# Performance work log

Hardware: AMD Instinct MI355X
Metric: run time of the kernel (lower is better)

The kernel has to match this reference:

```python
import jax, jax.numpy as jnp
import numpy as np

N_ATOMS = 131072
N_EDGES = 524288
N_MOLS = 2048
D = 128      # n_atom_basis
F = 128      # n_filters
G = 50       # n_gaussians
T = 3        # interaction blocks
CUTOFF = 5.0
LOG2 = float(np.log(2.0))


def ssp(x):
    # shifted softplus: ln(0.5*e^x + 0.5) = softplus(x) - ln 2
    return jax.nn.softplus(x) - LOG2


def setup_inputs() -> dict:
    key = jax.random.key(0)
    ks = jax.random.split(key, 20)
    s = 0.05
    z = jax.random.randint(ks[0], (N_ATOMS,), 1, 100, dtype=jnp.int32)
    xyz = jax.random.normal(ks[1], (N_ATOMS, 3), dtype=jnp.float32) * 3.0
    a0 = jax.random.randint(ks[2], (N_EDGES,), 0, N_ATOMS, dtype=jnp.int32)
    off = jax.random.randint(ks[3], (N_EDGES,), 1, N_ATOMS, dtype=jnp.int32)
    a = jnp.stack([a0, (a0 + off) % N_ATOMS], axis=1)  # distinct endpoints
    mol_id = jnp.sort(jax.random.randint(ks[4], (N_ATOMS,), 0, N_MOLS, dtype=jnp.int32))
    emb = (jax.random.normal(ks[5], (100, D)) * s).at[0].set(0.0)  # padding_idx=0
    return dict(
        xyz=xyz,
        emb=emb,
        fw1=jax.random.normal(ks[6], (T, G, F)) * s,
        fb1=jnp.zeros((T, F)),
        fw2=jax.random.normal(ks[7], (T, F, F)) * s,
        fb2=jnp.zeros((T, F)),
        win=jax.random.normal(ks[8], (T, D, F)) * s,
        wout1=jax.random.normal(ks[9], (T, F, D)) * s,
        bout1=jnp.zeros((T, D)),
        wout2=jax.random.normal(ks[10], (T, D, D)) * s,
        bout2=jnp.zeros((T, D)),
        wa1=jax.random.normal(ks[11], (D, D // 2)) * s,
        ba1=jnp.zeros((D // 2,)),
        wa2=jax.random.normal(ks[12], (D // 2, 1)) * s,
        ba2=jnp.zeros((1,)),
        z=z, a=a, mol_id=mol_id,
    )


def reference(xyz, emb, fw1, fb1, fw2, fb2, win, wout1, bout1, wout2, bout2,
              wa1, ba1, wa2, ba2, z, a, mol_id):
    r = emb[z]                                            # [N, D] atom embeddings
    # edge distances: e = ||xyz[a0] - xyz[a1]||  -> [E, 1]
    d = jnp.sqrt(((xyz[a[:, 0]] - xyz[a[:, 1]]) ** 2).sum(-1))[:, None]
    # Gaussian smearing on [0, cutoff]
    offsets = jnp.linspace(0.0, CUTOFF, G)
    width = offsets[1] - offsets[0]
    g = jnp.exp((-0.5 / width ** 2) * (d - offsets) ** 2)  # [E, G]
    # smooth cosine cutoff (cutoff_soft)
    C = 0.5 * (jnp.cos(d * jnp.pi / CUTOFF) + 1.0)          # [E, 1]
    for t in range(T):
        # continuous filter network on edge features
        W = ssp(g @ fw1[t] + fb1[t]) @ fw2[t] + fb2[t]      # [E, F]
        W = W * C
        h = r @ win[t]                                      # in2f, no bias [N, F]
        # symmetric gather-filter-scatter over undirected edge list
        y = jnp.zeros_like(h)
        y = y.at[a[:, 0]].add(h[a[:, 1]] * W)
        y = y.at[a[:, 1]].add(h[a[:, 0]] * W)
        dr = ssp(y @ wout1[t] + bout1[t]) @ wout2[t] + bout2[t]
        r = r + dr                                          # residual update
    # atomwise energy head
    r = ssp(r @ wa1 + ba1) @ wa2 + ba2                      # [N, 1]
    # per-molecule sum pooling (torch.split + sum)
    return jax.ops.segment_sum(r, mol_id, num_segments=N_MOLS)  # [N_MOLS, 1]
```

## Files before the change

kernel.cpp:

```cpp
#include <hip/hip_runtime.h>
#include <hip/hip_bf16.h>

#define N_ATOMS 131072
#define N_EDGES 524288
#define N_MOLS  2048
#define DD      128
#define FF      128
#define GG      50
#define TT      3

typedef __hip_bfloat16 bf16;
typedef __attribute__((ext_vector_type(8))) short short8;
typedef __attribute__((ext_vector_type(4))) float floatx4;

__device__ __forceinline__ float b2f(bf16 v) { return __bfloat162float(v); }
__device__ __forceinline__ bf16  f2b(float v) { return __float2bfloat16(v); }

__device__ __forceinline__ unsigned short f2bu(float f) {
    unsigned u = __float_as_uint(f);
    u += 0x7fff + ((u >> 16) & 1);
    return (unsigned short)(u >> 16);
}
__device__ __forceinline__ bf16 f2b_fast(float f) {
    union { unsigned short u; bf16 b; } c; c.u = f2bu(f); return c.b;
}
__device__ __forceinline__ unsigned int pk2(float lo, float hi) {
    return ((unsigned)f2bu(hi) << 16) | f2bu(lo);
}

__device__ __forceinline__ float2 up2(unsigned int u) {
    float2 f;
    f.x = __uint_as_float(u << 16);
    f.y = __uint_as_float(u & 0xffff0000u);
    return f;
}

__device__ __forceinline__ float sspf(float x) {
    float e = __expf(-fabsf(x));
    return fmaxf(x, 0.f) + __logf(1.f + e) - 0.69314718056f;
}

__device__ __forceinline__ void fma8(float* ac, uint4 wv, uint4 hv) {
    float2 w0 = up2(wv.x), h0 = up2(hv.x);
    float2 w1 = up2(wv.y), h1 = up2(hv.y);
    float2 w2 = up2(wv.z), h2 = up2(hv.z);
    float2 w3 = up2(wv.w), h3 = up2(hv.w);
    ac[0] = fmaf(w0.x, h0.x, ac[0]); ac[1] = fmaf(w0.y, h0.y, ac[1]);
    ac[2] = fmaf(w1.x, h1.x, ac[2]); ac[3] = fmaf(w1.y, h1.y, ac[3]);
    ac[4] = fmaf(w2.x, h2.x, ac[4]); ac[5] = fmaf(w2.y, h2.y, ac[5]);
    ac[6] = fmaf(w3.x, h3.x, ac[6]); ac[7] = fmaf(w3.y, h3.y, ac[7]);
}

template <int NCT>
__device__ __forceinline__ void mfma_half(const bf16* A, const bf16* B,
                                          floatx4 (&acc)[2][NCT],
                                          int kA, int wave, int q, int ln) {
#pragma unroll
    for (int k0 = 0; k0 < 64; k0 += 32) {
        short8 a0 = *(const short8*)(A + (wave * 32 + ln) * 136 + kA + k0 + q * 8);
        short8 a1 = *(const short8*)(A + (wave * 32 + 16 + ln) * 136 + kA + k0 + q * 8);
#pragma unroll
        for (int ct = 0; ct < NCT; ct++) {
            short8 b = *(const short8*)(B + (ct * 16 + ln) * 72 + k0 + q * 8);
            acc[0][ct] = __builtin_amdgcn_mfma_f32_16x16x32_bf16(a0, b, acc[0][ct], 0, 0, 0);
            acc[1][ct] = __builtin_amdgcn_mfma_f32_16x16x32_bf16(a1, b, acc[1][ct], 0, 0, 0);
        }
    }
}

template <int NCT>
__device__ __forceinline__ void mfma64(const bf16* A, const bf16* B,
                                       floatx4 (&acc)[NCT],
                                       int kA, int wave, int q, int ln) {
#pragma unroll
    for (int k0 = 0; k0 < 64; k0 += 32) {
        short8 a = *(const short8*)(A + (wave * 16 + ln) * 136 + kA + k0 + q * 8);
#pragma unroll
        for (int ct = 0; ct < NCT; ct++) {
            short8 b = *(const short8*)(B + (ct * 16 + ln) * 72 + k0 + q * 8);
            acc[ct] = __builtin_amdgcn_mfma_f32_16x16x32_bf16(a, b, acc[ct], 0, 0, 0);
        }
    }
}

__device__ __forceinline__ void stage_b(bf16* B, const bf16* WT, int k0,
                                        int nrows, int ldk, int tid) {
    for (int i = tid; i < nrows * 8; i += 256) {
        int n = i >> 3, kc = i & 7;
        *(short8*)(B + n * 72 + kc * 8) =
            *(const short8*)(WT + n * ldk + k0 + kc * 8);
    }
}

__global__ __launch_bounds__(256) void k_init(const float* __restrict__ emb,
                                              const int* __restrict__ z,
                                              float* __restrict__ r) {
    int idx = blockIdx.x * 256 + threadIdx.x;
    int atom = idx >> 7, col = idx & 127;
    r[idx] = emb[z[atom] * DD + col];
}

__global__ __launch_bounds__(256) void k_dist(const float* __restrict__ xyz,
                                              const int* __restrict__ a,
                                              float* __restrict__ dArr,
                                              float* __restrict__ cArr,
                                              float* __restrict__ molE) {
    int e = blockIdx.x * 256 + threadIdx.x;
    if (e < N_MOLS) molE[e] = 0.f;
    int A0 = a[2 * e], A1 = a[2 * e + 1];
    float dx = xyz[3 * A0]     - xyz[3 * A1];
    float dy = xyz[3 * A0 + 1] - xyz[3 * A1 + 1];
    float dz = xyz[3 * A0 + 2] - xyz[3 * A1 + 2];
    float d = sqrtf(dx * dx + dy * dy + dz * dz);
    dArr[e] = d;
    cArr[e] = 0.5f * (__cosf(d * 0.6283185307179586f) + 1.f);
}

__global__ __launch_bounds__(256) void k_wt(const float* __restrict__ fw1,
                                            const float* __restrict__ fw2,
                                            const float* __restrict__ win,
                                            const float* __restrict__ wout1,
                                            const float* __restrict__ wout2,
                                            const float* __restrict__ wa1,
                                            bf16* __restrict__ fw1T, bf16* __restrict__ fw2T,
                                            bf16* __restrict__ winT, bf16* __restrict__ wout1T,
                                            bf16* __restrict__ wout2T, bf16* __restrict__ wa1T) {
    int idx = blockIdx.x * 256 + threadIdx.x;
    if (idx < 3 * 128 * 64) {
        int t = idx / 8192, j = idx % 8192;
        int n = j >> 6, k = j & 63;
        fw1T[idx] = (k < GG) ? f2b(fw1[t * GG * FF + k * FF + n]) : f2b(0.f);
        return;
    }
    idx -= 3 * 128 * 64;
    if (idx < 3 * 16384) { int t = idx / 16384, j = idx % 16384; int n = j >> 7, k = j & 127;
        fw2T[idx] = f2b(fw2[t * 16384 + k * 128 + n]); return; }
    idx -= 3 * 16384;
    if (idx < 3 * 16384) { int t = idx / 16384, j = idx % 16384; int n = j >> 7, k = j & 127;
        winT[idx] = f2b(win[t * 16384 + k * 128 + n]); return; }
    idx -= 3 * 16384;
    if (idx < 3 * 16384) { int t = idx / 16384, j = idx % 16384; int n = j >> 7, k = j & 127;
        wout1T[idx] = f2b(wout1[t * 16384 + k * 128 + n]); return; }
    idx -= 3 * 16384;
    if (idx < 3 * 16384) { int t = idx / 16384, j = idx % 16384; int n = j >> 7, k = j & 127;
        wout2T[idx] = f2b(wout2[t * 16384 + k * 128 + n]); return; }
    idx -= 3 * 16384;
    if (idx < 64 * 128) { int n = idx >> 7, k = idx & 127;
        wa1T[idx] = f2b(wa1[k * 64 + n]); return; }
}

__global__ __launch_bounds__(256) void k_zero(int* __restrict__ p, int n) {
    int i = blockIdx.x * 256 + threadIdx.x;
    if (i < n) p[i] = 0;
}

__global__ __launch_bounds__(256) void k_count2(const int* __restrict__ a,
                                                int* __restrict__ cntA,
                                                int* __restrict__ cnt1,
                                                float* __restrict__ molE) {
    int e = blockIdx.x * 256 + threadIdx.x;
    if (e < N_MOLS) molE[e] = 0.f;
    atomicAdd(&cntA[a[2 * e]], 1);
    atomicAdd(&cnt1[a[2 * e + 1]], 1);
}

__global__ __launch_bounds__(256) void k_scan1(const int* __restrict__ counts,
                                               int* __restrict__ bsum) {
    __shared__ int red[256];
    int tid = threadIdx.x;
    int i0 = blockIdx.x * 512 + tid * 2;
    red[tid] = counts[i0] + counts[i0 + 1];
    __syncthreads();
    for (int off = 128; off > 0; off >>= 1) {
        if (tid < off) red[tid] += red[tid + off];
        __syncthreads();
    }
    if (tid == 0) bsum[blockIdx.x] = red[0];
}

__global__ __launch_bounds__(256) void k_scan2(int* __restrict__ bsum,
                                               int* __restrict__ ptr) {
    __shared__ int v[256];
    int tid = threadIdx.x;
    v[tid] = bsum[tid];
    __syncthreads();
    if (tid == 0) {
        int acc = 0;
        for (int i = 0; i < 256; i++) { int t = v[i]; v[i] = acc; acc += t; }
        ptr[N_ATOMS] = acc;
    }
    __syncthreads();
    bsum[tid] = v[tid];
}

__global__ __launch_bounds__(256) void k_scan3(int* __restrict__ counts,
                                               const int* __restrict__ bsum,
                                               int* __restrict__ ptr) {
    __shared__ int red[256];
    int tid = threadIdx.x;
    int i0 = blockIdx.x * 512 + tid * 2;
    int c0 = counts[i0], c1 = counts[i0 + 1];
    int s = c0 + c1;
    red[tid] = s;
    __syncthreads();
    for (int off = 1; off < 256; off <<= 1) {
        int t = (tid >= off) ? red[tid - off] : 0;
        __syncthreads();
        red[tid] += t;
        __syncthreads();
    }
    int base = bsum[blockIdx.x] + red[tid] - s;
    ptr[i0] = base;
    ptr[i0 + 1] = base + c0;
    counts[i0] = base;
    counts[i0 + 1] = base + c0;
}

__global__ __launch_bounds__(256) void k_permA(const float* __restrict__ xyz,
                                               const int* __restrict__ a,
                                               int* __restrict__ cursorA,
                                               int* __restrict__ cursor1,
                                               float* __restrict__ dAp,
                                               float* __restrict__ cAp,
                                               int* __restrict__ a1s,
                                               int* __restrict__ adj1) {
    int e = blockIdx.x * 256 + threadIdx.x;
    int A0 = a[2 * e], A1 = a[2 * e + 1];
    float dx = xyz[3 * A0]     - xyz[3 * A1];
    float dy = xyz[3 * A0 + 1] - xyz[3 * A1 + 1];
    float dz = xyz[3 * A0 + 2] - xyz[3 * A1 + 2];
    float d = sqrtf(dx * dx + dy * dy + dz * dz);
    int newe = atomicAdd(&cursorA[A0], 1);
    dAp[newe] = d;
    cAp[newe] = 0.5f * (__cosf(d * 0.6283185307179586f) + 1.f);
    a1s[newe] = A1;
    int slot = atomicAdd(&cursor1[A1], 1);
    adj1[2 * slot] = newe;
    adj1[2 * slot + 1] = A0;
}

struct SmemHE {
    bf16 A[64][136];
    bf16 B[128][72];
    float dS[64], cS[64], b1S[128], b2S[128];
};

__device__ __forceinline__ void h_part(SmemHE& sm, int blk,
                                       const float* __restrict__ r,
                                       const bf16* __restrict__ winT_t,
                                       bf16* __restrict__ h) {
    int tid = threadIdx.x, n0 = blk * 64;
    for (int i = tid; i < 64 * 32; i += 256) {
        int row = i >> 5, c4 = (i & 31) * 4;
        float4 v = *(const float4*)(r + (size_t)(n0 + row) * DD + c4);
        uint2 p; p.x = pk2(v.x, v.y); p.y = pk2(v.z, v.w);
        *(uint2*)(&sm.A[row][c4]) = p;
    }
    stage_b(&sm.B[0][0], winT_t, 0, 128, 128, tid);
    __syncthreads();
    int wave = tid >> 6, lane = tid & 63, q = lane >> 4, ln = lane & 15;
    floatx4 acc[8];
#pragma unroll
    for (int j = 0; j < 8; j++) acc[j] = (floatx4){0.f, 0.f, 0.f, 0.f};
    mfma64<8>(&sm.A[0][0], &sm.B[0][0], acc, 0, wave, q, ln);
    __syncthreads();
    stage_b(&sm.B[0][0], winT_t, 64, 128, 128, tid);
    __syncthreads();
    mfma64<8>(&sm.A[0][0], &sm.B[0][0], acc, 64, wave, q, ln);
#pragma unroll
    for (int ct = 0; ct < 8; ct++)
#pragma unroll
        for (int rg = 0; rg < 4; rg++) {
            int row = wave * 16 + q * 4 + rg, col = ct * 16 + ln;
            sm.A[row][col] = f2b_fast(acc[ct][rg]);
        }
    __syncthreads();
    for (int i = tid; i < 64 * 16; i += 256) {
        int row = i >> 4, seg = i & 15;
        *(uint4*)(h + (size_t)(n0 + row) * FF + seg * 8) =
            *(const uint4*)(&sm.A[row][seg * 8]);
    }
}

__device__ __forceinline__ void edge_part(SmemHE& sm, int blk,
                                          const float* __restrict__ dAp,
                                          const float* __restrict__ cAp,
                                          const bf16* __restrict__ fw1T_t,
                                          const float* __restrict__ fb1_t,
                                          const bf16* __restrict__ fw2T_t,
                                          const float* __restrict__ fb2_t,
                                          bf16* __restrict__ Wt) {
    int tid = threadIdx.x, e0 = blk * 64;
    if (tid < 64) { sm.dS[tid] = dAp[e0 + tid]; sm.cS[tid] = cAp[e0 + tid]; }
    if (tid < 128) { sm.b1S[tid] = fb1_t[tid]; sm.b2S[tid] = fb2_t[tid]; }
    stage_b(&sm.B[0][0], fw1T_t, 0, 128, 64, tid);
    __syncthreads();
    const float width = 5.0f / 49.0f;
    const float coeff = -0.5f / (width * width);
    for (int idx = tid; idx < 64 * 32; idx += 256) {
        int i = idx >> 5, kp = (idx & 31) * 2;
        float d = sm.dS[i];
        float t0 = d - (float)kp * width;
        float t1 = d - (float)(kp + 1) * width;
        float v0 = (kp < GG)     ? __expf(coeff * t0 * t0) : 0.f;
        float v1 = (kp + 1 < GG) ? __expf(coeff * t1 * t1) : 0.f;
        *(unsigned int*)(&sm.A[i][kp]) = pk2(v0, v1);
    }
    __syncthreads();
    int wave = tid >> 6, lane = tid & 63, q = lane >> 4, ln = lane & 15;
    floatx4 acc[8];
#pragma unroll
    for (int j = 0; j < 8; j++) acc[j] = (floatx4){0.f, 0.f, 0.f, 0.f};
    mfma64<8>(&sm.A[0][0], &sm.B[0][0], acc, 0, wave, q, ln);
#pragma unroll
    for (int ct = 0; ct < 8; ct++)
#pragma unroll
        for (int rg = 0; rg < 4; rg++) {
            int row = wave * 16 + q * 4 + rg, col = ct * 16 + ln;
            sm.A[row][col] = f2b_fast(sspf(acc[ct][rg] + sm.b1S[col]));
        }
    __syncthreads();
    stage_b(&sm.B[0][0], fw2T_t, 0, 128, 128, tid);
    __syncthreads();
#pragma unroll
    for (int j = 0; j < 8; j++) acc[j] = (floatx4){0.f, 0.f, 0.f, 0.f};
    mfma64<8>(&sm.A[0][0], &sm.B[0][0], acc, 0, wave, q, ln);
    __syncthreads();
    stage_b(&sm.B[0][0], fw2T_t, 64, 128, 128, tid);
    __syncthreads();
    mfma64<8>(&sm.A[0][0], &sm.B[0][0], acc, 64, wave, q, ln);
#pragma unroll
    for (int ct = 0; ct < 8; ct++)
#pragma unroll
        for (int rg = 0; rg < 4; rg++) {
            int row = wave * 16 + q * 4 + rg, col = ct * 16 + ln;
            sm.A[row][col] = f2b_fast((acc[ct][rg] + sm.b2S[col]) * sm.cS[row]);
        }
    __syncthreads();
    for (int i = tid; i < 64 * 16; i += 256) {
        int row = i >> 4, seg = i & 15;
        *(uint4*)(Wt + (size_t)(e0 + row) * FF + seg * 8) =
            *(const uint4*)(&sm.A[row][seg * 8]);
    }
}

__global__ __launch_bounds__(256, 4) void k_he(const float* __restrict__ r,
                                               const bf16* __restrict__ winT_t,
                                               bf16* __restrict__ h,
                                               const float* __restrict__ dAp,
                                               const float* __restrict__ cAp,
                                               const bf16* __restrict__ fw1T_t,
                                               const float* __restrict__ fb1_t,
                                               const bf16* __restrict__ fw2T_t,
                                               const float* __restrict__ fb2_t,
                                               bf16* __restrict__ Wt) {
    __shared__ SmemHE sm;
    int bi = blockIdx.x;
    if (bi % 5 == 0)
        h_part(sm, bi / 5, r, winT_t, h);
    else
        edge_part(sm, bi - bi / 5 - 1, dAp, cAp, fw1T_t, fb1_t, fw2T_t, fb2_t, Wt);
}

__global__ __launch_bounds__(256, 5) void k_gather_node64(const int* __restrict__ baseA,
                                                          const int* __restrict__ a1s,
                                                          const int* __restrict__ ptr1,
                                                          const int* __restrict__ adj1,
                                                          const bf16* __restrict__ Wt,
                                                          const bf16* __restrict__ h,
                                                          const bf16* __restrict__ wout1T_t,
                                                          const float* __restrict__ bo1_t,
                                                          const bf16* __restrict__ wout2T_t,
                                                          const float* __restrict__ bo2_t,
                                                          float* __restrict__ r) {
    __shared__ __align__(16) bf16 A[64][136];
    __shared__ __align__(16) bf16 B[64][72];
    __shared__ float b1S[128], b2S[128];
    int tid = threadIdx.x, n0 = blockIdx.x * 64;
    if (tid < 128) { b1S[tid] = bo1_t[tid]; b2S[tid] = bo2_t[tid]; }
    stage_b(&B[0][0], wout1T_t, 0, 64, 128, tid);
    int wave = tid >> 6, lane = tid & 63;
    int seg = lane & 15;
    int rg  = lane >> 4;
    for (int k = 0; k < 16; k++) {
        int row = wave * 16 + k;
        int atom = n0 + row;
        int s0 = baseA[atom] + rg, e0v = baseA[atom + 1];
        int s1 = ptr1[atom] + rg, e1v = ptr1[atom + 1];
        int o0 = (s0 < e0v) ? a1s[s0] : 0;
        int2 eo = (s1 < e1v) ? *(const int2*)(adj1 + 2 * s1) : make_int2(0, 0);
        float ac[8];
#pragma unroll
        for (int j = 0; j < 8; j++) ac[j] = 0.f;
        while (s0 < e0v || s1 < e1v) {
            bool p0 = s0 < e0v, p1 = s1 < e1v;
            uint4 wv0, hv0, wv1, hv1;
            if (p0) {
                wv0 = *(const uint4*)(Wt + (size_t)s0 * FF + seg * 8);
                hv0 = *(const uint4*)(h + (size_t)o0 * FF + seg * 8);
            }
            if (p1) {
                wv1 = *(const uint4*)(Wt + (size_t)eo.x * FF + seg * 8);
                hv1 = *(const uint4*)(h + (size_t)eo.y * FF + seg * 8);
            }
            int s0n = s0 + 4, s1n = s1 + 4;
            int o0n = (s0n < e0v) ? a1s[s0n] : 0;
            int2 eon = (s1n < e1v) ? *(const int2*)(adj1 + 2 * s1n) : make_int2(0, 0);
            if (p0) fma8(ac, wv0, hv0);
            if (p1) fma8(ac, wv1, hv1);
            s0 = s0n; s1 = s1n; o0 = o0n; eo = eon;
        }
#pragma unroll
        for (int j = 0; j < 8; j++) {
            float v = ac[j];
            v += __shfl_down(v, 32);
            v += __shfl_down(v, 16);
            ac[j] = v;
        }
        if (rg == 0) {
            uint4 o;
            o.x = pk2(ac[0], ac[1]);
            o.y = pk2(ac[2], ac[3]);
            o.z = pk2(ac[4], ac[5]);
            o.w = pk2(ac[6], ac[7]);
            *(uint4*)(&A[row][seg * 8]) = o;
        }
    }
    __syncthreads();
    int q = lane >> 4, ln = lane & 15;
    floatx4 acc[8];
#pragma unroll
    for (int j = 0; j < 8; j++) acc[j] = (floatx4){0.f, 0.f, 0.f, 0.f};
    mfma64<4>(&A[0][0], &B[0][0], *(floatx4(*)[4])(&acc[0]), 0, wave, q, ln);
    __syncthreads();
    stage_b(&B[0][0], wout1T_t + 64 * 128, 0, 64, 128, tid);
    __syncthreads();
    mfma64<4>(&A[0][0], &B[0][0], *(floatx4(*)[4])(&acc[4]), 0, wave, q, ln);
    __syncthreads();
    stage_b(&B[0][0], wout1T_t, 64, 64, 128, tid);
    __syncthreads();
    mfma64<4>(&A[0][0], &B[0][0], *(floatx4(*)[4])(&acc[0]), 64, wave, q, ln);
    __syncthreads();
    stage_b(&B[0][0], wout1T_t + 64 * 128, 64, 64, 128, tid);
    __syncthreads();
    mfma64<4>(&A[0][0], &B[0][0], *(floatx4(*)[4])(&acc[4]), 64, wave, q, ln);
#pragma unroll
    for (int cc = 0; cc < 8; cc++)
#pragma unroll
        for (int rgi = 0; rgi < 4; rgi++) {
            int row = wave * 16 + q * 4 + rgi;
            int col = (cc >> 2) * 64 + (cc & 3) * 16 + ln;
            A[row][col] = f2b_fast(sspf(acc[cc][rgi] + b1S[col]));
        }
    __syncthreads();
    stage_b(&B[0][0], wout2T_t, 0, 64, 128, tid);
    __syncthreads();
#pragma unroll
    for (int j = 0; j < 8; j++) acc[j] = (floatx4){0.f, 0.f, 0.f, 0.f};
    mfma64<4>(&A[0][0], &B[0][0], *(floatx4(*)[4])(&acc[0]), 0, wave, q, ln);
    __syncthreads();
    stage_b(&B[0][0], wout2T_t + 64 * 128, 0, 64, 128, tid);
    __syncthreads();
    mfma64<4>(&A[0][0], &B[0][0], *(floatx4(*)[4])(&acc[4]), 0, wave, q, ln);
    __syncthreads();
    stage_b(&B[0][0], wout2T_t, 64, 64, 128, tid);
    __syncthreads();
    mfma64<4>(&A[0][0], &B[0][0], *(floatx4(*)[4])(&acc[0]), 64, wave, q, ln);
    __syncthreads();
    stage_b(&B[0][0], wout2T_t + 64 * 128, 64, 64, 128, tid);
    __syncthreads();
    mfma64<4>(&A[0][0], &B[0][0], *(floatx4(*)[4])(&acc[4]), 64, wave, q, ln);
#pragma unroll
    for (int cc = 0; cc < 8; cc++)
#pragma unroll
        for (int rgi = 0; rgi < 4; rgi++) {
            int row = wave * 16 + q * 4 + rgi;
            int col = (cc >> 2) * 64 + (cc & 3) * 16 + ln;
            size_t off = (size_t)(n0 + row) * DD + col;
            r[off] += acc[cc][rgi] + b2S[col];
        }
}

__global__ __launch_bounds__(256) void k_h(const float* __restrict__ r,
                                           const bf16* __restrict__ winT_t,
                                           bf16* __restrict__ h,
                                           float* __restrict__ y) {
    __shared__ __align__(16) bf16 A[128][136];
    __shared__ __align__(16) bf16 B[128][72];
    int tid = threadIdx.x, n0 = blockIdx.x * 128;
    for (int i = tid; i < 128 * 32; i += 256) {
        int row = i >> 5, c4 = (i & 31) * 4;
        float4 v = *(const float4*)(r + (size_t)(n0 + row) * DD + c4);
        A[row][c4]     = f2b(v.x);
        A[row][c4 + 1] = f2b(v.y);
        A[row][c4 + 2] = f2b(v.z);
        A[row][c4 + 3] = f2b(v.w);
        *(float4*)(y + (size_t)(n0 + row) * FF + c4) = (float4){0.f, 0.f, 0.f, 0.f};
    }
    stage_b(&B[0][0], winT_t, 0, 128, 128, tid);
    __syncthreads();
    int wave = tid >> 6, lane = tid & 63, q = lane >> 4, ln = lane & 15;
    floatx4 acc[2][8];
#pragma unroll
    for (int i = 0; i < 2; i++)
#pragma unroll
        for (int j = 0; j < 8; j++) acc[i][j] = (floatx4){0.f, 0.f, 0.f, 0.f};
    mfma_half<8>(&A[0][0], &B[0][0], acc, 0, wave, q, ln);
    __syncthreads();
    stage_b(&B[0][0], winT_t, 64, 128, 128, tid);
    __syncthreads();
    mfma_half<8>(&A[0][0], &B[0][0], acc, 64, wave, q, ln);
#pragma unroll
    for (int rt = 0; rt < 2; rt++)
#pragma unroll
        for (int ct = 0; ct < 8; ct++)
#pragma unroll
            for (int rg = 0; rg < 4; rg++) {
                int row = wave * 32 + rt * 16 + q * 4 + rg, col = ct * 16 + ln;
                h[(size_t)(n0 + row) * FF + col] = f2b(acc[rt][ct][rg]);
            }
}

__global__ __launch_bounds__(256) void k_edge(const float* __restrict__ dArr,
                                              const float* __restrict__ cArr,
                                              const int* __restrict__ a,
                                              const bf16* __restrict__ fw1T_t,
                                              const float* __restrict__ fb1_t,
                                              const bf16* __restrict__ fw2T_t,
                                              const float* __restrict__ fb2_t,
                                              const bf16* __restrict__ h,
                                              float* __restrict__ y) {
    __shared__ __align__(16) bf16 A[128][136];
    __shared__ __align__(16) bf16 B[128][72];
    __shared__ float dS[128], cS[128], b1S[128], b2S[128];
    __shared__ int a0S[128], a1S[128];
    int tid = threadIdx.x, e0 = blockIdx.x * 128;
    if (tid < 128) {
        int e = e0 + tid;
        dS[tid] = dArr[e]; cS[tid] = cArr[e];
        a0S[tid] = a[2 * e]; a1S[tid] = a[2 * e + 1];
        b1S[tid] = fb1_t[tid]; b2S[tid] = fb2_t[tid];
    }
    stage_b(&B[0][0], fw1T_t, 0, 128, 64, tid);
    __syncthreads();
    const float width = 5.0f / 49.0f;
    const float coeff = -0.5f / (width * width);
    for (int idx = tid; idx < 128 * 64; idx += 256) {
        int i = idx >> 6, k = idx & 63;
        float v = 0.f;
        if (k < GG) { float t = dS[i] - (float)k * width; v = __expf(coeff * t * t); }
        A[i][k] = f2b(v);
    }
    __syncthreads();
    int wave = tid >> 6, lane = tid & 63, q = lane >> 4, ln = lane & 15;
    floatx4 acc[2][8];
#pragma unroll
    for (int i = 0; i < 2; i++)
#pragma unroll
        for (int j = 0; j < 8; j++) acc[i][j] = (floatx4){0.f, 0.f, 0.f, 0.f};
    mfma_half<8>(&A[0][0], &B[0][0], acc, 0, wave, q, ln);
#pragma unroll
    for (int rt = 0; rt < 2; rt++)
#pragma unroll
        for (int ct = 0; ct < 8; ct++)
#pragma unroll
            for (int rg = 0; rg < 4; rg++) {
                int row = wave * 32 + rt * 16 + q * 4 + rg, col = ct * 16 + ln;
                A[row][col] = f2b(sspf(acc[rt][ct][rg] + b1S[col]));
            }
    __syncthreads();
    stage_b(&B[0][0], fw2T_t, 0, 128, 128, tid);
    __syncthreads();
#pragma unroll
    for (int i = 0; i < 2; i++)
#pragma unroll
        for (int j = 0; j < 8; j++) acc[i][j] = (floatx4){0.f, 0.f, 0.f, 0.f};
    mfma_half<8>(&A[0][0], &B[0][0], acc, 0, wave, q, ln);
    __syncthreads();
    stage_b(&B[0][0], fw2T_t, 64, 128, 128, tid);
    __syncthreads();
    mfma_half<8>(&A[0][0], &B[0][0], acc, 64, wave, q, ln);
#pragma unroll
    for (int rt = 0; rt < 2; rt++)
#pragma unroll
        for (int ct = 0; ct < 8; ct++)
#pragma unroll
            for (int rg = 0; rg < 4; rg++) {
                int row = wave * 32 + rt * 16 + q * 4 + rg, col = ct * 16 + ln;
                float w = (acc[rt][ct][rg] + b2S[col]) * cS[row];
                int A0 = a0S[row], A1 = a1S[row];
                float h0 = b2f(h[A0 * FF + col]);
                float h1 = b2f(h[A1 * FF + col]);
                atomicAdd(&y[A0 * FF + col], h1 * w);
                atomicAdd(&y[A1 * FF + col], h0 * w);
            }
}

__global__ __launch_bounds__(256) void k_node(const float* __restrict__ y,
                                              const bf16* __restrict__ wout1T_t,
                                              const float* __restrict__ bo1_t,
                                              const bf16* __restrict__ wout2T_t,
                                              const float* __restrict__ bo2_t,
                                              float* __restrict__ r) {
    __shared__ __align__(16) bf16 A[128][136];
    __shared__ __align__(16) bf16 B[128][72];
    __shared__ float b1S[128], b2S[128];
    int tid = threadIdx.x, n0 = blockIdx.x * 128;
    if (tid < 128) { b1S[tid] = bo1_t[tid]; b2S[tid] = bo2_t[tid]; }
    for (int idx = tid; idx < 128 * 128; idx += 256) {
        int row = idx >> 7, col = idx & 127;
        A[row][col] = f2b(y[(size_t)(n0 + row) * FF + col]);
    }
    stage_b(&B[0][0], wout1T_t, 0, 128, 128, tid);
    __syncthreads();
    int wave = tid >> 6, lane = tid & 63, q = lane >> 4, ln = lane & 15;
    floatx4 acc[2][8];
#pragma unroll
    for (int i = 0; i < 2; i++)
#pragma unroll
        for (int j = 0; j < 8; j++) acc[i][j] = (floatx4){0.f, 0.f, 0.f, 0.f};
    mfma_half<8>(&A[0][0], &B[0][0], acc, 0, wave, q, ln);
    __syncthreads();
    stage_b(&B[0][0], wout1T_t, 64, 128, 128, tid);
    __syncthreads();
    mfma_half<8>(&A[0][0], &B[0][0], acc, 64, wave, q, ln);
#pragma unroll
    for (int rt = 0; rt < 2; rt++)
#pragma unroll
        for (int ct = 0; ct < 8; ct++)
#pragma unroll
            for (int rg = 0; rg < 4; rg++) {
                int row = wave * 32 + rt * 16 + q * 4 + rg, col = ct * 16 + ln;
                A[row][col] = f2b(sspf(acc[rt][ct][rg] + b1S[col]));
            }
    __syncthreads();
    stage_b(&B[0][0], wout2T_t, 0, 128, 128, tid);
    __syncthreads();
#pragma unroll
    for (int i = 0; i < 2; i++)
#pragma unroll
        for (int j = 0; j < 8; j++) acc[i][j] = (floatx4){0.f, 0.f, 0.f, 0.f};
    mfma_half<8>(&A[0][0], &B[0][0], acc, 0, wave, q, ln);
    __syncthreads();
    stage_b(&B[0][0], wout2T_t, 64, 128, 128, tid);
    __syncthreads();
    mfma_half<8>(&A[0][0], &B[0][0], acc, 64, wave, q, ln);
#pragma unroll
    for (int rt = 0; rt < 2; rt++)
#pragma unroll
        for (int ct = 0; ct < 8; ct++)
#pragma unroll
            for (int rg = 0; rg < 4; rg++) {
                int row = wave * 32 + rt * 16 + q * 4 + rg, col = ct * 16 + ln;
                size_t off = (size_t)(n0 + row) * DD + col;
                r[off] += acc[rt][ct][rg] + b2S[col];
            }
}

__global__ __launch_bounds__(256) void k_head(const float* __restrict__ r,
                                              const bf16* __restrict__ wa1T,
                                              const float* __restrict__ ba1,
                                              const float* __restrict__ wa2,
                                              const float* __restrict__ ba2,
                                              const int* __restrict__ mol,
                                              float* __restrict__ molE) {
    __shared__ __align__(16) bf16 A[128][136];
    __shared__ __align__(16) bf16 B[64][72];
    __shared__ __align__(16) bf16 U[128][72];
    __shared__ float wa2S[64], ba1S[64];
    int tid = threadIdx.x, n0 = blockIdx.x * 128;
    if (tid < 64) { wa2S[tid] = wa2[tid]; ba1S[tid] = ba1[tid]; }
    for (int i = tid; i < 128 * 32; i += 256) {
        int row = i >> 5, c4 = (i & 31) * 4;
        float4 v = *(const float4*)(r + (size_t)(n0 + row) * DD + c4);
        uint2 p; p.x = pk2(v.x, v.y); p.y = pk2(v.z, v.w);
        *(uint2*)(&A[row][c4]) = p;
    }
    stage_b(&B[0][0], wa1T, 0, 64, 128, tid);
    __syncthreads();
    int wave = tid >> 6, lane = tid & 63, q = lane >> 4, ln = lane & 15;
    floatx4 acc[2][4];
#pragma unroll
    for (int i = 0; i < 2; i++)
#pragma unroll
        for (int j = 0; j < 4; j++) acc[i][j] = (floatx4){0.f, 0.f, 0.f, 0.f};
    mfma_half<4>(&A[0][0], &B[0][0], acc, 0, wave, q, ln);
    __syncthreads();
    stage_b(&B[0][0], wa1T, 64, 64, 128, tid);
    __syncthreads();
    mfma_half<4>(&A[0][0], &B[0][0], acc, 64, wave, q, ln);
#pragma unroll
    for (int rt = 0; rt < 2; rt++)
#pragma unroll
        for (int ct = 0; ct < 4; ct++)
#pragma unroll
            for (int rg = 0; rg < 4; rg++) {
                int row = wave * 32 + rt * 16 + q * 4 + rg, col = ct * 16 + ln;
                U[row][col] = f2b_fast(acc[rt][ct][rg] + ba1S[col]);
            }
    __syncthreads();
    if (tid < 128) {
        float s = ba2[0];
#pragma unroll
        for (int j = 0; j < 64; j++) s += sspf(b2f(U[tid][j])) * wa2S[j];
        atomicAdd(&molE[mol[n0 + tid]], s);
    }
}

__global__ __launch_bounds__(256) void k_out(const float* __restrict__ molE,
                                             float* __restrict__ out) {
    int i = blockIdx.x * 256 + threadIdx.x;
    out[i] = molE[i];
}

extern "C" void kernel_launch(void* const* d_in, const int* in_sizes, int n_in,
                              void* d_out, int out_size, void* d_ws, size_t ws_size,
                              hipStream_t stream) {
    const float* xyz   = (const float*)d_in[0];
    const float* emb   = (const float*)d_in[1];
    const float* fw1   = (const float*)d_in[2];
    const float* fb1   = (const float*)d_in[3];
    const float* fw2   = (const float*)d_in[4];
    const float* fb2   = (const float*)d_in[5];
    const float* win   = (const float*)d_in[6];
    const float* wout1 = (const float*)d_in[7];
    const float* bout1 = (const float*)d_in[8];
    const float* wout2 = (const float*)d_in[9];
    const float* bout2 = (const float*)d_in[10];
    const float* wa1   = (const float*)d_in[11];
    const float* ba1   = (const float*)d_in[12];
    const float* wa2   = (const float*)d_in[13];
    const float* ba2   = (const float*)d_in[14];
    const int*  z     = (const int*)d_in[15];
    const int*  a     = (const int*)d_in[16];
    const int*  mol   = (const int*)d_in[17];

    char* ws = (char*)d_ws;
    float* r    = (float*)ws; ws += (size_t)N_ATOMS * DD * 4;
    bf16*  h    = (bf16*) ws; ws += (size_t)N_ATOMS * FF * 2;
    float* molE = (float*)ws; ws += (size_t)N_MOLS * 4;
    float* dAp  = (float*)ws; ws += (size_t)N_EDGES * 4;
    float* cAp  = (float*)ws; ws += (size_t)N_EDGES * 4;
    bf16*  fw1T   = (bf16*)ws; ws += 3 * 128 * 64 * 2;
    bf16*  fw2T   = (bf16*)ws; ws += 3 * 128 * 128 * 2;
    bf16*  winT   = (bf16*)ws; ws += 3 * 128 * 128 * 2;
    bf16*  wout1T = (bf16*)ws; ws += 3 * 128 * 128 * 2;
    bf16*  wout2T = (bf16*)ws; ws += 3 * 128 * 128 * 2;
    bf16*  wa1T   = (bf16*)ws; ws += 64 * 128 * 2;
    char*  csr_base = ws;
    int*   baseA   = (int*)ws; ws += 524320;
    int*   ptr1    = (int*)ws; ws += 524320;
    int*   cursorA = (int*)ws; ws += (size_t)N_ATOMS * 4;
    int*   cursor1 = (int*)ws; ws += (size_t)N_ATOMS * 4;
    int*   a1s     = (int*)ws; ws += (size_t)N_EDGES * 4;
    int*   adj1    = (int*)ws; ws += (size_t)2 * N_EDGES * 4;
    int*   bsumA   = (int*)ws; ws += 1024;
    int*   bsum1   = (int*)ws; ws += 1024;
    bf16*  Wt      = (bf16*)ws; ws += (size_t)N_EDGES * FF * 2;
    size_t need = (size_t)(ws - (char*)d_ws);

    k_init<<<N_ATOMS * DD / 256, 256, 0, stream>>>(emb, z, r);
    k_wt<<<896, 256, 0, stream>>>(fw1, fw2, win, wout1, wout2, wa1,
                                  fw1T, fw2T, winT, wout1T, wout2T, wa1T);

    if (ws_size >= need) {
        k_zero<<<(N_ATOMS + 255) / 256, 256, 0, stream>>>(cursorA, N_ATOMS);
        k_zero<<<(N_ATOMS + 255) / 256, 256, 0, stream>>>(cursor1, N_ATOMS);
        k_count2<<<N_EDGES / 256, 256, 0, stream>>>(a, cursorA, cursor1, molE);
        k_scan1<<<256, 256, 0, stream>>>(cursorA, bsumA);
        k_scan2<<<1, 256, 0, stream>>>(bsumA, baseA);
        k_scan3<<<256, 256, 0, stream>>>(cursorA, bsumA, baseA);
        k_scan1<<<256, 256, 0, stream>>>(cursor1, bsum1);
        k_scan2<<<1, 256, 0, stream>>>(bsum1, ptr1);
        k_scan3<<<256, 256, 0, stream>>>(cursor1, bsum1, ptr1);
        k_permA<<<N_EDGES / 256, 256, 0, stream>>>(xyz, a, cursorA, cursor1,
                                                   dAp, cAp, a1s, adj1);
        for (int t = 0; t < TT; t++) {
            k_he<<<N_ATOMS / 64 + N_EDGES / 64, 256, 0, stream>>>(
                r, winT + t * 16384, h, dAp, cAp,
                fw1T + t * 8192, fb1 + t * FF,
                fw2T + t * 16384, fb2 + t * FF, Wt);
            k_gather_node64<<<N_ATOMS / 64, 256, 0, stream>>>(
                baseA, a1s, ptr1, adj1, Wt, h,
                wout1T + t * 16384, bout1 + t * DD,
                wout2T + t * 16384, bout2 + t * DD, r);
        }
    } else {
        float* y = (float*)csr_base;
        k_dist<<<N_EDGES / 256, 256, 0, stream>>>(xyz, a, dAp, cAp, molE);
        for (int t = 0; t < TT; t++) {
            k_h<<<N_ATOMS / 128, 256, 0, stream>>>(r, winT + t * 16384, h, y);
            k_edge<<<N_EDGES / 128, 256, 0, stream>>>(dAp, cAp, a,
                                                      fw1T + t * 8192, fb1 + t * FF,
                                                      fw2T + t * 16384, fb2 + t * FF, h, y);
            k_node<<<N_ATOMS / 128, 256, 0, stream>>>(y, wout1T + t * 16384, bout1 + t * DD,
                                                      wout2T + t * 16384, bout2 + t * DD, r);
        }
    }
    k_head<<<N_ATOMS / 128, 256, 0, stream>>>(r, wa1T, ba1, wa2, ba2, mol, molE);
    k_out<<<N_MOLS / 256, 256, 0, stream>>>(molE, (float*)d_out);
}
```

Measured before the change: 1.054 ms.

## Store residual state in bf16 and process two atoms per gather iteration

The residual atom state r is now held in bf16 instead of fp32, which halves its memory traffic in init, the h GEMM, the node update and the head, and removes the per-kernel fp32-to-bf16 packing. The gather/node kernel also processes two atoms at once in its neighbor loop, interleaving their edge streams to raise memory-level parallelism. The cost is that residual accumulation is rounded to bf16 on every block, which may affect accuracy, and that the unrolled loop uses more registers.

After: 993.9 us. 1.06x faster.

```diff
diff --git a/kernel.cpp b/kernel.cpp
--- a/kernel.cpp
+++ b/kernel.cpp
@@ -94,10 +94,16 @@
 
 __global__ __launch_bounds__(256) void k_init(const float* __restrict__ emb,
                                               const int* __restrict__ z,
-                                              float* __restrict__ r) {
+                                              bf16* __restrict__ rb) {
     int idx = blockIdx.x * 256 + threadIdx.x;
-    int atom = idx >> 7, col = idx & 127;
-    r[idx] = emb[z[atom] * DD + col];
+    int atom = idx >> 4, seg = idx & 15;
+    const float* src = emb + (size_t)z[atom] * DD + seg * 8;
+    float4 v0 = *(const float4*)(src);
+    float4 v1 = *(const float4*)(src + 4);
+    uint4 o;
+    o.x = pk2(v0.x, v0.y); o.y = pk2(v0.z, v0.w);
+    o.z = pk2(v1.x, v1.y); o.w = pk2(v1.z, v1.w);
+    *(uint4*)(rb + (size_t)atom * DD + seg * 8) = o;
 }
 
 __global__ __launch_bounds__(256) void k_dist(const float* __restrict__ xyz,
@@ -246,15 +252,14 @@
 };
 
 __device__ __forceinline__ void h_part(SmemHE& sm, int blk,
-                                       const float* __restrict__ r,
+                                       const bf16* __restrict__ rb,
                                        const bf16* __restrict__ winT_t,
                                        bf16* __restrict__ h) {
     int tid = threadIdx.x, n0 = blk * 64;
-    for (int i = tid; i < 64 * 32; i += 256) {
-        int row = i >> 5, c4 = (i & 31) * 4;
-        float4 v = *(const float4*)(r + (size_t)(n0 + row) * DD + c4);
-        uint2 p; p.x = pk2(v.x, v.y); p.y = pk2(v.z, v.w);
-        *(uint2*)(&sm.A[row][c4]) = p;
+    for (int i = tid; i < 64 * 16; i += 256) {
+        int row = i >> 4, seg = i & 15;
+        *(uint4*)(&sm.A[row][seg * 8]) =
+            *(const uint4*)(rb + (size_t)(n0 + row) * DD + seg * 8);
     }
     stage_b(&sm.B[0][0], winT_t, 0, 128, 128, tid);
     __syncthreads();
@@ -344,7 +349,7 @@
     }
 }
 
-__global__ __launch_bounds__(256, 4) void k_he(const float* __restrict__ r,
+__global__ __launch_bounds__(256, 4) void k_he(const bf16* __restrict__ rb,
                                                const bf16* __restrict__ winT_t,
                                                bf16* __restrict__ h,
                                                const float* __restrict__ dAp,
@@ -357,7 +362,7 @@
     __shared__ SmemHE sm;
     int bi = blockIdx.x;
     if (bi % 5 == 0)
-        h_part(sm, bi / 5, r, winT_t, h);
+        h_part(sm, bi / 5, rb, winT_t, h);
     else
         edge_part(sm, bi - bi / 5 - 1, dAp, cAp, fw1T_t, fb1_t, fw2T_t, fb2_t, Wt);
 }
@@ -372,7 +377,7 @@
                                                           const float* __restrict__ bo1_t,
                                                           const bf16* __restrict__ wout2T_t,
                                                           const float* __restrict__ bo2_t,
-                                                          float* __restrict__ r) {
+                                                          bf16* __restrict__ rb) {
     __shared__ __align__(16) bf16 A[64][136];
     __shared__ __align__(16) bf16 B[64][72];
     __shared__ float b1S[128], b2S[128];
@@ -382,48 +387,71 @@
     int wave = tid >> 6, lane = tid & 63;
     int seg = lane & 15;
     int rg  = lane >> 4;
-    for (int k = 0; k < 16; k++) {
-        int row = wave * 16 + k;
-        int atom = n0 + row;
-        int s0 = baseA[atom] + rg, e0v = baseA[atom + 1];
-        int s1 = ptr1[atom] + rg, e1v = ptr1[atom + 1];
-        int o0 = (s0 < e0v) ? a1s[s0] : 0;
-        int2 eo = (s1 < e1v) ? *(const int2*)(adj1 + 2 * s1) : make_int2(0, 0);
-        float ac[8];
-#pragma unroll
-        for (int j = 0; j < 8; j++) ac[j] = 0.f;
-        while (s0 < e0v || s1 < e1v) {
-            bool p0 = s0 < e0v, p1 = s1 < e1v;
-            uint4 wv0, hv0, wv1, hv1;
-            if (p0) {
-                wv0 = *(const uint4*)(Wt + (size_t)s0 * FF + seg * 8);
-                hv0 = *(const uint4*)(h + (size_t)o0 * FF + seg * 8);
-            }
-            if (p1) {
-                wv1 = *(const uint4*)(Wt + (size_t)eo.x * FF + seg * 8);
-                hv1 = *(const uint4*)(h + (size_t)eo.y * FF + seg * 8);
-            }
-            int s0n = s0 + 4, s1n = s1 + 4;
-            int o0n = (s0n < e0v) ? a1s[s0n] : 0;
-            int2 eon = (s1n < e1v) ? *(const int2*)(adj1 + 2 * s1n) : make_int2(0, 0);
-            if (p0) fma8(ac, wv0, hv0);
-            if (p1) fma8(ac, wv1, hv1);
-            s0 = s0n; s1 = s1n; o0 = o0n; eo = eon;
+    for (int k = 0; k < 16; k += 2) {
+        int rowA = wave * 16 + k;
+        int atomA = n0 + rowA;
+        int2 b01 = *(const int2*)(baseA + atomA);
+        int b2v = baseA[atomA + 2];
+        int2 p01 = *(const int2*)(ptr1 + atomA);
+        int p2v = ptr1[atomA + 2];
+        int sA0 = b01.x + rg, eA0v = b01.y;
+        int sB0 = b01.y + rg, eB0v = b2v;
+        int sA1 = p01.x + rg, eA1v = p01.y;
+        int sB1 = p01.y + rg, eB1v = p2v;
+        int oA = (sA0 < eA0v) ? a1s[sA0] : 0;
+        int oB = (sB0 < eB0v) ? a1s[sB0] : 0;
+        int2 eoA = (sA1 < eA1v) ? *(const int2*)(adj1 + 2 * sA1) : make_int2(0, 0);
+        int2 eoB = (sB1 < eB1v) ? *(const int2*)(adj1 + 2 * sB1) : make_int2(0, 0);
+        float acA[8], acB[8];
+#pragma unroll
+        for (int j = 0; j < 8; j++) { acA[j] = 0.f; acB[j] = 0.f; }
+        while ((sA0 < eA0v) | (sA1 < eA1v) | (sB0 < eB0v) | (sB1 < eB1v)) {
+            bool pA0 = sA0 < eA0v, pA1 = sA1 < eA1v;
+            bool pB0 = sB0 < eB0v, pB1 = sB1 < eB1v;
+            uint4 wvA0, hvA0, wvA1, hvA1, wvB0, hvB0, wvB1, hvB1;
+            if (pA0) {
+                wvA0 = *(const uint4*)(Wt + (size_t)sA0 * FF + seg * 8);
+                hvA0 = *(const uint4*)(h + (size_t)oA * FF + seg * 8);
+            }
+            if (pA1) {
+                wvA1 = *(const uint4*)(Wt + (size_t)eoA.x * FF + seg * 8);
+                hvA1 = *(const uint4*)(h + (size_t)eoA.y * FF + seg * 8);
+            }
+            if (pB0) {
+                wvB0 = *(const uint4*)(Wt + (size_t)sB0 * FF + seg * 8);
+                hvB0 = *(const uint4*)(h + (size_t)oB * FF + seg * 8);
+            }
+            if (pB1) {
+                wvB1 = *(const uint4*)(Wt + (size_t)eoB.x * FF + seg * 8);
+                hvB1 = *(const uint4*)(h + (size_t)eoB.y * FF + seg * 8);
+            }
+            int sA0n = sA0 + 4, sA1n = sA1 + 4, sB0n = sB0 + 4, sB1n = sB1 + 4;
+            int oAn = (sA0n < eA0v) ? a1s[sA0n] : 0;
+            int oBn = (sB0n < eB0v) ? a1s[sB0n] : 0;
+            int2 eoAn = (sA1n < eA1v) ? *(const int2*)(adj1 + 2 * sA1n) : make_int2(0, 0);
+            int2 eoBn = (sB1n < eB1v) ? *(const int2*)(adj1 + 2 * sB1n) : make_int2(0, 0);
+            if (pA0) fma8(acA, wvA0, hvA0);
+            if (pA1) fma8(acA, wvA1, hvA1);
+            if (pB0) fma8(acB, wvB0, hvB0);
+            if (pB1) fma8(acB, wvB1, hvB1);
+            sA0 = sA0n; sA1 = sA1n; sB0 = sB0n; sB1 = sB1n;
+            oA = oAn; oB = oBn; eoA = eoAn; eoB = eoBn;
         }
 #pragma unroll
         for (int j = 0; j < 8; j++) {
-            float v = ac[j];
-            v += __shfl_down(v, 32);
-            v += __shfl_down(v, 16);
-            ac[j] = v;
+            float vA = acA[j], vB = acB[j];
+            vA += __shfl_down(vA, 32); vB += __shfl_down(vB, 32);
+            vA += __shfl_down(vA, 16); vB += __shfl_down(vB, 16);
+            acA[j] = vA; acB[j] = vB;
         }
         if (rg == 0) {
-            uint4 o;
-            o.x = pk2(ac[0], ac[1]);
-            o.y = pk2(ac[2], ac[3]);
-            o.z = pk2(ac[4], ac[5]);
-            o.w = pk2(ac[6], ac[7]);
-            *(uint4*)(&A[row][seg * 8]) = o;
+            uint4 oU;
+            oU.x = pk2(acA[0], acA[1]); oU.y = pk2(acA[2], acA[3]);
+            oU.z = pk2(acA[4], acA[5]); oU.w = pk2(acA[6], acA[7]);
+            *(uint4*)(&A[rowA][seg * 8]) = oU;
+            oU.x = pk2(acB[0], acB[1]); oU.y = pk2(acB[2], acB[3]);
+            oU.z = pk2(acB[4], acB[5]); oU.w = pk2(acB[6], acB[7]);
+            *(uint4*)(&A[rowA + 1][seg * 8]) = oU;
         }
     }
     __syncthreads();
@@ -477,25 +505,23 @@
             int row = wave * 16 + q * 4 + rgi;
             int col = (cc >> 2) * 64 + (cc & 3) * 16 + ln;
             size_t off = (size_t)(n0 + row) * DD + col;
-            r[off] += acc[cc][rgi] + b2S[col];
-        }
-}
-
-__global__ __launch_bounds__(256) void k_h(const float* __restrict__ r,
+            rb[off] = f2b_fast(b2f(rb[off]) + acc[cc][rgi] + b2S[col]);
+        }
+}
+
+__global__ __launch_bounds__(256) void k_h(const bf16* __restrict__ rb,
                                            const bf16* __restrict__ winT_t,
                                            bf16* __restrict__ h,
                                            float* __restrict__ y) {
     __shared__ __align__(16) bf16 A[128][136];
     __shared__ __align__(16) bf16 B[128][72];
     int tid = threadIdx.x, n0 = blockIdx.x * 128;
-    for (int i = tid; i < 128 * 32; i += 256) {
-        int row = i >> 5, c4 = (i & 31) * 4;
-        float4 v = *(const float4*)(r + (size_t)(n0 + row) * DD + c4);
-        A[row][c4]     = f2b(v.x);
-        A[row][c4 + 1] = f2b(v.y);
-        A[row][c4 + 2] = f2b(v.z);
-        A[row][c4 + 3] = f2b(v.w);
-        *(float4*)(y + (size_t)(n0 + row) * FF + c4) = (float4){0.f, 0.f, 0.f, 0.f};
+    for (int i = tid; i < 128 * 16; i += 256) {
+        int row = i >> 4, seg = i & 15;
+        *(uint4*)(&A[row][seg * 8]) =
+            *(const uint4*)(rb + (size_t)(n0 + row) * DD + seg * 8);
+        *(float4*)(y + (size_t)(n0 + row) * FF + seg * 8) = (float4){0.f, 0.f, 0.f, 0.f};
+        *(float4*)(y + (size_t)(n0 + row) * FF + seg * 8 + 4) = (float4){0.f, 0.f, 0.f, 0.f};
     }
     stage_b(&B[0][0], winT_t, 0, 128, 128, tid);
     __syncthreads();
@@ -601,7 +627,7 @@
                                               const float* __restrict__ bo1_t,
                                               const bf16* __restrict__ wout2T_t,
                                               const float* __restrict__ bo2_t,
-                                              float* __restrict__ r) {
+                                              bf16* __restrict__ rb) {
     __shared__ __align__(16) bf16 A[128][136];
     __shared__ __align__(16) bf16 B[128][72];
     __shared__ float b1S[128], b2S[128];
@@ -653,11 +679,11 @@
             for (int rg = 0; rg < 4; rg++) {
                 int row = wave * 32 + rt * 16 + q * 4 + rg, col = ct * 16 + ln;
                 size_t off = (size_t)(n0 + row) * DD + col;
-                r[off] += acc[rt][ct][rg] + b2S[col];
-            }
-}
-
-__global__ __launch_bounds__(256) void k_head(const float* __restrict__ r,
+                rb[off] = f2b_fast(b2f(rb[off]) + acc[rt][ct][rg] + b2S[col]);
+            }
+}
+
+__global__ __launch_bounds__(256) void k_head(const bf16* __restrict__ rb,
                                               const bf16* __restrict__ wa1T,
                                               const float* __restrict__ ba1,
                                               const float* __restrict__ wa2,
@@ -670,11 +696,10 @@
     __shared__ float wa2S[64], ba1S[64];
     int tid = threadIdx.x, n0 = blockIdx.x * 128;
     if (tid < 64) { wa2S[tid] = wa2[tid]; ba1S[tid] = ba1[tid]; }
-    for (int i = tid; i < 128 * 32; i += 256) {
-        int row = i >> 5, c4 = (i & 31) * 4;
-        float4 v = *(const float4*)(r + (size_t)(n0 + row) * DD + c4);
-        uint2 p; p.x = pk2(v.x, v.y); p.y = pk2(v.z, v.w);
-        *(uint2*)(&A[row][c4]) = p;
+    for (int i = tid; i < 128 * 16; i += 256) {
+        int row = i >> 4, seg = i & 15;
+        *(uint4*)(&A[row][seg * 8]) =
+            *(const uint4*)(rb + (size_t)(n0 + row) * DD + seg * 8);
     }
     stage_b(&B[0][0], wa1T, 0, 64, 128, tid);
     __syncthreads();
@@ -736,7 +761,7 @@
     const int*  mol   = (const int*)d_in[17];
 
     char* ws = (char*)d_ws;
-    float* r    = (float*)ws; ws += (size_t)N_ATOMS * DD * 4;
+    bf16*  rb   = (bf16*) ws; ws += (size_t)N_ATOMS * DD * 2;
     bf16*  h    = (bf16*) ws; ws += (size_t)N_ATOMS * FF * 2;
     float* molE = (float*)ws; ws += (size_t)N_MOLS * 4;
     float* dAp  = (float*)ws; ws += (size_t)N_EDGES * 4;
@@ -759,7 +784,7 @@
     bf16*  Wt      = (bf16*)ws; ws += (size_t)N_EDGES * FF * 2;
     size_t need = (size_t)(ws - (char*)d_ws);
 
-    k_init<<<N_ATOMS * DD / 256, 256, 0, stream>>>(emb, z, r);
+    k_init<<<N_ATOMS * 16 / 256, 256, 0, stream>>>(emb, z, rb);
     k_wt<<<896, 256, 0, stream>>>(fw1, fw2, win, wout1, wout2, wa1,
                                   fw1T, fw2T, winT, wout1T, wout2T, wa1T);
 
@@ -777,26 +802,26 @@
                                                    dAp, cAp, a1s, adj1);
         for (int t = 0; t < TT; t++) {
             k_he<<<N_ATOMS / 64 + N_EDGES / 64, 256, 0, stream>>>(
-                r, winT + t * 16384, h, dAp, cAp,
+                rb, winT + t * 16384, h, dAp, cAp,
                 fw1T + t * 8192, fb1 + t * FF,
                 fw2T + t * 16384, fb2 + t * FF, Wt);
             k_gather_node64<<<N_ATOMS / 64, 256, 0, stream>>>(
                 baseA, a1s, ptr1, adj1, Wt, h,
                 wout1T + t * 16384, bout1 + t * DD,
-                wout2T + t * 16384, bout2 + t * DD, r);
+                wout2T + t * 16384, bout2 + t * DD, rb);
         }
     } else {
         float* y = (float*)csr_base;
         k_dist<<<N_EDGES / 256, 256, 0, stream>>>(xyz, a, dAp, cAp, molE);
         for (int t = 0; t < TT; t++) {
-            k_h<<<N_ATOMS / 128, 256, 0, stream>>>(r, winT + t * 16384, h, y);
+            k_h<<<N_ATOMS / 128, 256, 0, stream>>>(rb, winT + t * 16384, h, y);
             k_edge<<<N_EDGES / 128, 256, 0, stream>>>(dAp, cAp, a,
                                                       fw1T + t * 8192, fb1 + t * FF,
                                                       fw2T + t * 16384, fb2 + t * FF, h, y);
             k_node<<<N_ATOMS / 128, 256, 0, stream>>>(y, wout1T + t * 16384, bout1 + t * DD,
-                                                      wout2T + t * 16384, bout2 + t * DD, r);
-        }
-    }
-    k_head<<<N_ATOMS / 128, 256, 0, stream>>>(r, wa1T, ba1, wa2, ba2, mol, molE);
+                                                      wout2T + t * 16384, bout2 + t * DD, rb);
+        }
+    }
+    k_head<<<N_ATOMS / 128, 256, 0, stream>>>(rb, wa1T, ba1, wa2, ba2, mol, molE);
     k_out<<<N_MOLS / 256, 256, 0, stream>>>(molE, (float*)d_out);
 }
```
